# Optimization experiments

Measured on AMD Instinct MI355X. Metric: run time of the kernel, lower is better.

The kernel has to match this reference:

```python
import jax, jax.numpy as jnp
import numpy as np

# Problem sizes: batch(+heads), seq (m=n), head dim, nonzeros per row
B, M, N, K, R = 8, 4096, 4096, 64, 128
NNZ = M * R


def setup_inputs() -> dict:
    key = jax.random.key(0)
    k1, k2, k3, k4 = jax.random.split(key, 4)
    # Uniform CSR: R nonzeros per row, columns sorted within each row.
    row_offsets = jnp.arange(M + 1, dtype=jnp.int32) * R
    column_indices = jax.random.randint(k4, (M, R), 0, N, dtype=jnp.int32)
    column_indices = jnp.sort(column_indices, axis=1).reshape(NNZ)
    # diffsort(row_offsets): row ids sorted by descending row length (load balancing,
    # does not affect the math).
    diffs = row_offsets[1:] - row_offsets[:-1]
    row_indices = jnp.argsort(-diffs).astype(jnp.int32)
    q3d = jax.random.normal(k1, (B, M, K), dtype=jnp.float32)
    k3d = jax.random.normal(k2, (B, N, K), dtype=jnp.float32)
    v3d = jax.random.normal(k3, (B, N, K), dtype=jnp.float32)
    # `values` is only an output buffer for sddmm in the original; contents unused.
    values = jnp.zeros((B, NNZ), dtype=jnp.float32)
    return {
        "row_indices": row_indices,
        "row_offsets": row_offsets,
        "column_indices": column_indices,
        "q3d": q3d,
        "k3d": k3d,
        "v3d": v3d,
        "values": values,
    }


def reference(row_indices, row_offsets, column_indices, q3d, k3d, v3d, values):
    m = row_offsets.shape[0] - 1
    nnz = column_indices.shape[0]
    # Row id of each CSR nonzero.
    row_ids = jnp.searchsorted(
        row_offsets, jnp.arange(nnz, dtype=row_offsets.dtype), side="right"
    ) - 1
    cols = column_indices

    # SDDMM: logits[b, e] = <Q[b, row(e), :], K[b, col(e), :]>  -> [B, nnz]
    logits = jnp.einsum("bed,bed->be", q3d[:, row_ids, :], k3d[:, cols, :])

    def attend_one(lg_b, v_b):
        # Sparse per-row softmax over the nonzeros of each row.
        mx = jax.ops.segment_max(lg_b, row_ids, num_segments=m)
        ex = jnp.exp(lg_b - mx[row_ids])
        den = jax.ops.segment_sum(ex, row_ids, num_segments=m)
        w = ex / den[row_ids]  # [nnz]
        # SPMM: out[i, :] = sum_{e in row i} w[e] * V[col(e), :]
        return jax.ops.segment_sum(w[:, None] * v_b[cols, :], row_ids, num_segments=m)

    return jax.vmap(attend_one)(logits, v3d)  # [B, M, K]
```

## Files before the change

kernel.cpp:

```cpp
#include <hip/hip_runtime.h>

#define Bc 8
#define Mc 4096
#define Nc 4096
#define Kc 64
#define Rc 128

typedef _Float16 h16;
typedef h16 h16x2 __attribute__((ext_vector_type(2)));
typedef h16 h16x4 __attribute__((ext_vector_type(4)));
typedef h16 h16x8 __attribute__((ext_vector_type(8)));

__global__ __launch_bounds__(256) void cvt_fp16(
    const float4* __restrict__ K4, const float4* __restrict__ V4,
    h16x4* __restrict__ Kh4, h16x4* __restrict__ Vh4)
{
    const int n4 = Bc * Nc * Kc / 4;
    int i = blockIdx.x * 256 + threadIdx.x;
    const float4* src; h16x4* dst; int idx;
    if (i < n4) { src = K4; dst = Kh4; idx = i; }
    else        { src = V4; dst = Vh4; idx = i - n4; }
    float4 v = src[idx];
    h16x4 o = { (h16)v.x, (h16)v.y, (h16)v.z, (h16)v.w };
    dst[idx] = o;
}

__global__ __launch_bounds__(256) void sattn_kernel(
    const int* __restrict__ cols,
    const float* __restrict__ Q,
    const h16* __restrict__ Kh,
    const h16* __restrict__ Vh,
    float* __restrict__ out)
{
    const int b   = blockIdx.x & 7;
    const int row = blockIdx.x >> 3;
    const int t   = threadIdx.x;
    const int g   = t >> 3;
    const int ln  = t & 7;

    __shared__ float s_w[Rc];
    __shared__ __align__(16) float s_part[32][Kc];
    __shared__ __align__(16) float s_red[4][Kc];
    __shared__ float s_invden;

    int col4[4];
    #pragma unroll
    for (int p = 0; p < 4; ++p) col4[p] = cols[row * Rc + p * 32 + g];

    const float4* qp = (const float4*)(Q + (((unsigned)b * Mc + row) << 6) + ln * 8);
    float4 q0 = qp[0], q1 = qp[1];
    h16x2 qh[4];
    qh[0] = h16x2{ (h16)q0.x, (h16)q0.y };
    qh[1] = h16x2{ (h16)q0.z, (h16)q0.w };
    qh[2] = h16x2{ (h16)q1.x, (h16)q1.y };
    qh[3] = h16x2{ (h16)q1.z, (h16)q1.w };

    h16x8 kv[4];
    #pragma unroll
    for (int p = 0; p < 4; ++p)
        kv[p] = *(const h16x8*)(Kh + ((((unsigned)b * Nc + col4[p]) << 6) + ln * 8));

    #pragma unroll
    for (int p = 0; p < 4; ++p) {
        float acc = 0.f;
        #pragma unroll
        for (int j = 0; j < 4; ++j) {
            h16x2 kj = { kv[p][2 * j], kv[p][2 * j + 1] };
#if defined(__has_builtin)
#if __has_builtin(__builtin_amdgcn_fdot2)
            acc = __builtin_amdgcn_fdot2(qh[j], kj, acc, false);
#else
            acc += (float)qh[j].x * (float)kj.x + (float)qh[j].y * (float)kj.y;
#endif
#else
            acc += (float)qh[j].x * (float)kj.x + (float)qh[j].y * (float)kj.y;
#endif
        }
        acc += __shfl_xor(acc, 1, 64);
        acc += __shfl_xor(acc, 2, 64);
        acc += __shfl_xor(acc, 4, 64);
        if (ln == 0) s_w[p * 32 + g] = acc;
    }

    h16x8 vv[4];
    #pragma unroll
    for (int p = 0; p < 4; ++p)
        vv[p] = *(const h16x8*)(Vh + ((((unsigned)b * Nc + col4[p]) << 6) + ln * 8));

    __syncthreads();

    if (t < 64) {
        float l0 = s_w[t], l1 = s_w[t + 64];
        float m = fmaxf(l0, l1);
        #pragma unroll
        for (int o = 32; o; o >>= 1) m = fmaxf(m, __shfl_xor(m, o, 64));
        float e0 = __expf(l0 - m), e1 = __expf(l1 - m);
        s_w[t] = e0; s_w[t + 64] = e1;
        float s = e0 + e1;
        #pragma unroll
        for (int o = 32; o; o >>= 1) s += __shfl_xor(s, o, 64);
        if (t == 0) s_invden = 1.0f / s;
    }
    __syncthreads();

    float acc8[8] = {0.f,0.f,0.f,0.f,0.f,0.f,0.f,0.f};
    #pragma unroll
    for (int p = 0; p < 4; ++p) {
        const float w = s_w[p * 32 + g];
        #pragma unroll
        for (int j = 0; j < 8; ++j)
            acc8[j] = fmaf((float)vv[p][j], w, acc8[j]);
    }
    *(float4*)&s_part[g][ln * 8]     = *(float4*)&acc8[0];
    *(float4*)&s_part[g][ln * 8 + 4] = *(float4*)&acc8[4];
    __syncthreads();

    {
        const int k = t & 63, qq = t >> 6;
        float r = 0.f;
        #pragma unroll
        for (int j = 0; j < 8; ++j) r += s_part[qq * 8 + j][k];
        s_red[qq][k] = r;
    }
    __syncthreads();
    if (t < 64) {
        float r = (s_red[0][t] + s_red[1][t]) + (s_red[2][t] + s_red[3][t]);
        out[(((unsigned)b * Mc + row) << 6) + t] = r * s_invden;
    }
}

extern "C" void kernel_launch(void* const* d_in, const int* in_sizes, int n_in,
                              void* d_out, int out_size, void* d_ws, size_t ws_size,
                              hipStream_t stream) {
    const int*   cols = (const int*)d_in[2];
    const float* Q    = (const float*)d_in[3];
    const float* Km   = (const float*)d_in[4];
    const float* Vm   = (const float*)d_in[5];
    float* out = (float*)d_out;

    h16* Kh = (h16*)d_ws;
    h16* Vh = Kh + (size_t)Bc * Nc * Kc;

    const int n4 = Bc * Nc * Kc / 4;
    cvt_fp16<<<dim3(2 * n4 / 256), dim3(256), 0, stream>>>(
        (const float4*)Km, (const float4*)Vm, (h16x4*)Kh, (h16x4*)Vh);
    sattn_kernel<<<dim3(Bc * Mc), dim3(256), 0, stream>>>(cols, Q, Kh, Vh, out);
}
```

Measured before the change: 143.8 us.

## Stream K/V column tiles through LDS with online softmax, 128 rows per block

Each block now handles 128 rows of one batch. It walks all of K and V in 256-column tiles staged into padded shared memory, and each 8-lane group consumes the sorted column indices that fall in the current tile. The softmax becomes an online (running max and sum) formulation, which removes the per-row block reductions and several syncs. The aim is to replace scattered global gathers with coalesced tile loads reused across rows. The cost is that every block streams the full K and V per batch, dense traffic of 4096 columns per 128 rows against 128x128 gathered columns, plus many syncs and serial per-group loops with divergence.

```diff
diff --git a/kernel.cpp b/kernel.cpp
--- a/kernel.cpp
+++ b/kernel.cpp
@@ -5,6 +5,11 @@
 #define Nc 4096
 #define Kc 64
 #define Rc 128
+#define TILE 256
+#define NT (Nc / TILE)
+#define RPB 128
+#define THREADS 1024
+#define KSTRIDE 72
 
 typedef _Float16 h16;
 typedef h16 h16x2 __attribute__((ext_vector_type(2)));
@@ -25,108 +30,110 @@
     dst[idx] = o;
 }
 
-__global__ __launch_bounds__(256) void sattn_kernel(
+__global__ __launch_bounds__(THREADS, 4) void sattn_kernel(
     const int* __restrict__ cols,
     const float* __restrict__ Q,
     const h16* __restrict__ Kh,
     const h16* __restrict__ Vh,
     float* __restrict__ out)
 {
-    const int b   = blockIdx.x & 7;
-    const int row = blockIdx.x >> 3;
-    const int t   = threadIdx.x;
-    const int g   = t >> 3;
-    const int ln  = t & 7;
+    const int b     = blockIdx.x & 7;
+    const int chunk = blockIdx.x >> 3;
+    const int t     = threadIdx.x;
+    const int g     = t >> 3;
+    const int ln    = t & 7;
+    const int laneid = t & 63;
+    const int gbase  = laneid & 56;
 
-    __shared__ float s_w[Rc];
-    __shared__ __align__(16) float s_part[32][Kc];
-    __shared__ __align__(16) float s_red[4][Kc];
-    __shared__ float s_invden;
+    __shared__ __align__(16) h16 s_k[TILE * KSTRIDE];
+    __shared__ __align__(16) h16 s_v[TILE * KSTRIDE];
 
-    int col4[4];
-    #pragma unroll
-    for (int p = 0; p < 4; ++p) col4[p] = cols[row * Rc + p * 32 + g];
+    const int row = chunk * RPB + g;
+    const int* colbase = cols + row * Rc;
 
-    const float4* qp = (const float4*)(Q + (((unsigned)b * Mc + row) << 6) + ln * 8);
-    float4 q0 = qp[0], q1 = qp[1];
+    const float* qp = Q + (((size_t)b * Mc + row) << 6) + ln * 8;
+    float4 q0 = *(const float4*)qp, q1 = *(const float4*)(qp + 4);
     h16x2 qh[4];
     qh[0] = h16x2{ (h16)q0.x, (h16)q0.y };
     qh[1] = h16x2{ (h16)q0.z, (h16)q0.w };
     qh[2] = h16x2{ (h16)q1.x, (h16)q1.y };
     qh[3] = h16x2{ (h16)q1.z, (h16)q1.w };
 
-    h16x8 kv[4];
-    #pragma unroll
-    for (int p = 0; p < 4; ++p)
-        kv[p] = *(const h16x8*)(Kh + ((((unsigned)b * Nc + col4[p]) << 6) + ln * 8));
+    float mrun = -1e30f, lrun = 0.f;
+    float acc8[8] = {0.f,0.f,0.f,0.f,0.f,0.f,0.f,0.f};
+    int p = 0;
 
-    #pragma unroll
-    for (int p = 0; p < 4; ++p) {
-        float acc = 0.f;
+    for (int tile = 0; tile < NT; ++tile) {
+        const int c0   = tile * TILE;
+        const int cend = c0 + TILE;
+
+        __syncthreads();
         #pragma unroll
-        for (int j = 0; j < 4; ++j) {
-            h16x2 kj = { kv[p][2 * j], kv[p][2 * j + 1] };
-#if defined(__has_builtin)
-#if __has_builtin(__builtin_amdgcn_fdot2)
-            acc = __builtin_amdgcn_fdot2(qh[j], kj, acc, false);
-#else
-            acc += (float)qh[j].x * (float)kj.x + (float)qh[j].y * (float)kj.y;
-#endif
-#else
-            acc += (float)qh[j].x * (float)kj.x + (float)qh[j].y * (float)kj.y;
-#endif
+        for (int i = 0; i < 2; ++i) {
+            const int c  = t + i * 1024;
+            const int r  = c >> 3;
+            const int l8 = c & 7;
+            const size_t goff = ((((size_t)b * Nc) + c0 + r) << 6) + l8 * 8;
+            *(h16x8*)&s_k[r * KSTRIDE + l8 * 8] = *(const h16x8*)(Kh + goff);
+            *(h16x8*)&s_v[r * KSTRIDE + l8 * 8] = *(const h16x8*)(Vh + goff);
         }
-        acc += __shfl_xor(acc, 1, 64);
-        acc += __shfl_xor(acc, 2, 64);
-        acc += __shfl_xor(acc, 4, 64);
-        if (ln == 0) s_w[p * 32 + g] = acc;
+        __syncthreads();
+
+        for (;;) {
+            const int myp   = p + ln;
+            const int mycol = (myp < Rc) ? colbase[myp] : 0x7fffffff;
+            const bool valid = mycol < cend;
+            unsigned long long bal = __ballot(valid);
+            const int cnt = __popcll((bal >> gbase) & 0xFFull);
+            if (cnt == 0) break;
+
+            float mylogit = 0.f;
+            float mchunk  = -1e30f;
+            for (int j = 0; j < cnt; ++j) {
+                const int colj = __shfl(mycol, gbase | j, 64);
+                const h16x8 kv = *(const h16x8*)&s_k[(colj - c0) * KSTRIDE + ln * 8];
+                float d = 0.f;
+                d = __builtin_amdgcn_fdot2(qh[0], h16x2{kv[0], kv[1]}, d, false);
+                d = __builtin_amdgcn_fdot2(qh[1], h16x2{kv[2], kv[3]}, d, false);
+                d = __builtin_amdgcn_fdot2(qh[2], h16x2{kv[4], kv[5]}, d, false);
+                d = __builtin_amdgcn_fdot2(qh[3], h16x2{kv[6], kv[7]}, d, false);
+                d += __shfl_xor(d, 1, 64);
+                d += __shfl_xor(d, 2, 64);
+                d += __shfl_xor(d, 4, 64);
+                if (ln == j) mylogit = d;
+                mchunk = fmaxf(mchunk, d);
+            }
+
+            const float mnew  = fmaxf(mrun, mchunk);
+            const float alpha = __expf(mrun - mnew);
+            lrun *= alpha;
+            #pragma unroll
+            for (int k = 0; k < 8; ++k) acc8[k] *= alpha;
+            mrun = mnew;
+
+            for (int j = 0; j < cnt; ++j) {
+                const int src  = gbase | j;
+                const float lg = __shfl(mylogit, src, 64);
+                const int colj = __shfl(mycol, src, 64);
+                const float w  = __expf(lg - mrun);
+                lrun += w;
+                const h16x8 vv = *(const h16x8*)&s_v[(colj - c0) * KSTRIDE + ln * 8];
+                #pragma unroll
+                for (int k = 0; k < 8; ++k)
+                    acc8[k] = fmaf((float)vv[k], w, acc8[k]);
+            }
+
+            p += cnt;
+            if (cnt < 8) break;
+        }
     }
 
-    h16x8 vv[4];
-    #pragma unroll
-    for (int p = 0; p < 4; ++p)
-        vv[p] = *(const h16x8*)(Vh + ((((unsigned)b * Nc + col4[p]) << 6) + ln * 8));
-
-    __syncthreads();
-
-    if (t < 64) {
-        float l0 = s_w[t], l1 = s_w[t + 64];
-        float m = fmaxf(l0, l1);
-        #pragma unroll
-        for (int o = 32; o; o >>= 1) m = fmaxf(m, __shfl_xor(m, o, 64));
-        float e0 = __expf(l0 - m), e1 = __expf(l1 - m);
-        s_w[t] = e0; s_w[t + 64] = e1;
-        float s = e0 + e1;
-        #pragma unroll
-        for (int o = 32; o; o >>= 1) s += __shfl_xor(s, o, 64);
-        if (t == 0) s_invden = 1.0f / s;
-    }
-    __syncthreads();
-
-    float acc8[8] = {0.f,0.f,0.f,0.f,0.f,0.f,0.f,0.f};
-    #pragma unroll
-    for (int p = 0; p < 4; ++p) {
-        const float w = s_w[p * 32 + g];
-        #pragma unroll
-        for (int j = 0; j < 8; ++j)
-            acc8[j] = fmaf((float)vv[p][j], w, acc8[j]);
-    }
-    *(float4*)&s_part[g][ln * 8]     = *(float4*)&acc8[0];
-    *(float4*)&s_part[g][ln * 8 + 4] = *(float4*)&acc8[4];
-    __syncthreads();
-
-    {
-        const int k = t & 63, qq = t >> 6;
-        float r = 0.f;
-        #pragma unroll
-        for (int j = 0; j < 8; ++j) r += s_part[qq * 8 + j][k];
-        s_red[qq][k] = r;
-    }
-    __syncthreads();
-    if (t < 64) {
-        float r = (s_red[0][t] + s_red[1][t]) + (s_red[2][t] + s_red[3][t]);
-        out[(((unsigned)b * Mc + row) << 6) + t] = r * s_invden;
-    }
+    const float inv = 1.0f / lrun;
+    float4 o0 = { acc8[0]*inv, acc8[1]*inv, acc8[2]*inv, acc8[3]*inv };
+    float4 o1 = { acc8[4]*inv, acc8[5]*inv, acc8[6]*inv, acc8[7]*inv };
+    float* op = out + (((size_t)b * Mc + row) << 6) + ln * 8;
+    *(float4*)op       = o0;
+    *(float4*)(op + 4) = o1;
 }
 
 extern "C" void kernel_launch(void* const* d_in, const int* in_sizes, int n_in,
@@ -144,5 +151,5 @@
     const int n4 = Bc * Nc * Kc / 4;
     cvt_fp16<<<dim3(2 * n4 / 256), dim3(256), 0, stream>>>(
         (const float4*)Km, (const float4*)Vm, (h16x4*)Kh, (h16x4*)Vh);
-    sattn_kernel<<<dim3(Bc * Mc), dim3(256), 0, stream>>>(cols, Q, Kh, Vh, out);
+    sattn_kernel<<<dim3(Bc * (Mc / RPB)), dim3(THREADS), 0, stream>>>(cols, Q, Kh, Vh, out);
 }
```

Result: slower. 215.8 us (+50.0%).
